# Kernel optimization log

Measured on AMD Instinct MI355X. Metric: run time of the kernel, lower is better.

## Reference

```python
import jax, jax.numpy as jnp
import numpy as np

D, H, C = 128, 128, 10
N, M, T = 256, 128, 128
DELTA = 1.0
SIGMA2 = 1.0
JITTER = 1e-3


def _net(params, x):
    # x: (D,) -> (C,)   2-hidden-layer tanh MLP (the `network` of NTKSVGP)
    W1, b1, W2, b2, W3, b3 = params
    h = jnp.tanh(x @ W1 + b1)
    h = jnp.tanh(h @ W2 + b2)
    return h @ W3 + b3


def _flat_jac(params, X):
    # per-sample jacobian wrt all params, flattened over params: (B, C, P)
    jac = jax.vmap(lambda x: jax.jacrev(_net)(params, x))(X)
    leaves = jax.tree_util.tree_leaves(jac)
    return jnp.concatenate([j.reshape(j.shape[0], j.shape[1], -1) for j in leaves], axis=-1)


def _forward(X, Y, Z, X_test, W1, b1, W2, b2, W3, b3):
    params = (W1, b1, W2, b2, W3, b3)
    scale = 1.0 / (DELTA * N)  # build_ntk: 1/(delta*num_data)

    Jx = _flat_jac(params, X)       # (N, C, P)
    Jz = _flat_jac(params, Z)       # (M, C, P)
    Jt = _flat_jac(params, X_test)  # (T, C, P)

    Kzx = jnp.einsum('mcp,ncp->cmn', Jz, Jx) * scale   # (C, M, N)
    Kzz = jnp.einsum('mcp,kcp->cmk', Jz, Jz) * scale   # (C, M, M)

    # Gaussian likelihood duals: beta = 2*Hessian = I/sigma2, alpha = -d nll/df = (Y-F)/sigma2
    F = jax.vmap(_net, in_axes=(None, 0))(params, X)   # (N, C)
    beta_diag = jnp.ones_like(F) / SIGMA2              # (N, C)
    alpha = (Y - F) / SIGMA2
    Lam = alpha + F * beta_diag                        # calc_lambda

    # beta_u = Kzx diag(beta) Kzx^T ; Lambda_u = Kzx Lambda
    beta_u = jnp.einsum('cmn,nc,ckn->cmk', Kzx, beta_diag, Kzx)  # (C, M, M)
    Lambda_u = jnp.einsum('cmn,nc->cm', Kzx, Lam)                # (C, M)

    Iz = jnp.eye(M, dtype=Kzz.dtype)
    Kzz_j = Kzz + JITTER * Iz
    KzzB = Kzz_j + beta_u + JITTER * Iz
    alpha_u = jnp.linalg.solve(KzzB, Lambda_u[..., None])[..., 0]  # (C, M)

    # predict_from_sparse_duals (full_cov=False branch)
    Lm = jnp.linalg.cholesky(Kzz_j)  # lower, batched over C
    Lb = jnp.linalg.cholesky(KzzB)
    Kxz = jnp.einsum('tcp,mcp->ctm', Jt, Jz) * scale  # (C, T, M)
    Kxx_diag = jnp.einsum('tcp,tcp->ct', Jt, Jt) * scale  # (C, T)

    f_mean = jnp.einsum('ctm,cm->tc', Kxz, alpha_u)   # (T, C)
    Kzxt = jnp.swapaxes(Kxz, -1, -2)                  # (C, M, T)
    Am = jax.scipy.linalg.solve_triangular(Lm, Kzxt, lower=True)
    Ab = jax.scipy.linalg.solve_triangular(Lb, Kzxt, lower=True)
    f_var = Kxx_diag - jnp.sum(Am * Am, axis=-2) + jnp.sum(Ab * Ab, axis=-2)  # (C, T)
    return jnp.stack([f_mean, f_var.T])  # (2, T, C)


def setup_inputs() -> dict:
    key = jax.random.key(0)
    ks = jax.random.split(key, 8)
    return {
        'X': jax.random.normal(ks[0], (N, D), jnp.float32),
        'Y': jax.random.normal(ks[1], (N, C), jnp.float32),
        'Z': jax.random.normal(ks[2], (M, D), jnp.float32),
        'X_test': jax.random.normal(ks[3], (T, D), jnp.float32),
        'W1': jax.random.normal(ks[4], (D, H), jnp.float32) / np.sqrt(D),
        'b1': jnp.zeros((H,), jnp.float32),
        'W2': jax.random.normal(ks[5], (H, H), jnp.float32) / np.sqrt(H),
        'b2': jnp.zeros((H,), jnp.float32),
        'W3': jax.random.normal(ks[6], (H, C), jnp.float32) / np.sqrt(H),
        'b3': jnp.zeros((C,), jnp.float32),
    }


def reference(X, Y, Z, X_test, W1, b1, W2, b2, W3, b3):
    return _forward(X, Y, Z, X_test, W1, b1, W2, b2, W3, b3)
```

## Files before the change

### kernel.cpp

```cpp
#include <hip/hip_runtime.h>

#define H 128
#define DD 128
#define CC 10
#define NX 256
#define MZ 128
#define TN 128
#define S_TOT 512
#define SCALE (1.0f/256.0f)
#define JIT 1e-3f
#define INV_S2 1.0f

#define OFF_XS    0u
#define OFF_A1    (OFF_XS   + S_TOT*DD)
#define OFF_A2    (OFF_A1   + S_TOT*H)
#define OFF_G1    (OFF_A2   + S_TOT*H)
#define OFF_G2    (OFF_G1   + S_TOT*CC*H)
#define OFF_W2T   (OFF_G2   + S_TOT*CC*H)
#define OFF_BASE  (OFF_W2T  + H*H)
#define BASE_ZX   0u
#define BASE_ZZ   (3u*MZ*NX)
#define BASE_TZ   (3u*MZ*NX + 3u*MZ*MZ)
#define OFF_KZX   (OFF_BASE + 3u*MZ*NX + 3u*MZ*MZ + 3u*TN*MZ)
#define OFF_KZZ   (OFF_KZX  + CC*MZ*NX)
#define OFF_KXZ   (OFF_KZZ  + CC*MZ*MZ)
#define OFF_KZZJ  (OFF_KXZ  + CC*TN*MZ)
#define OFF_KZZB  (OFF_KZZJ + CC*MZ*MZ)
#define OFF_LAMU  (OFF_KZZB + CC*MZ*MZ)
#define OFF_LC    (OFF_LAMU + CC*MZ)
#define OFF_INVD  (OFF_LC   + 2u*CC*MZ*MZ)
#define OFF_YLAM  (OFF_INVD + 2u*CC*MZ)

__global__ __launch_bounds__(128) void k_w2t(const float* __restrict__ W2, float* __restrict__ W2T,
                                             float* __restrict__ LamU) {
  int k = blockIdx.x, h = threadIdx.x;
  W2T[k*H + h] = W2[h*H + k];
  if (k < CC) LamU[k*MZ + h] = 0.0f;
}

__global__ __launch_bounds__(128) void k_features(
    const float* __restrict__ X, const float* __restrict__ Z, const float* __restrict__ Xt,
    const float* __restrict__ W1, const float* __restrict__ b1,
    const float* __restrict__ W2, const float* __restrict__ b2,
    const float* __restrict__ W3, const float* __restrict__ W2T,
    float* __restrict__ XS, float* __restrict__ A1, float* __restrict__ A2,
    float* __restrict__ G1, float* __restrict__ G2, float* __restrict__ out)
{
  int s = blockIdx.x, h = threadIdx.x;
  const float* xin = (s < NX) ? X + s*DD : (s < NX+MZ ? Z + (s-NX)*DD : Xt + (s-NX-MZ)*DD);
  __shared__ float xs[DD], a1s[H], g2s[CC*H];
  __shared__ float red[2];
  float xv = xin[h];
  xs[h] = xv; XS[s*DD + h] = xv;
  __syncthreads();
  float acc = b1[h];
  #pragma unroll 4
  for (int d0 = 0; d0 < DD; ++d0) acc += xs[d0] * W1[d0*H + h];
  float a1 = tanhf(acc);
  a1s[h] = a1; A1[s*H + h] = a1;
  __syncthreads();
  acc = b2[h];
  #pragma unroll 4
  for (int d0 = 0; d0 < H; ++d0) acc += a1s[d0] * W2[d0*H + h];
  float a2 = tanhf(acc);
  A2[s*H + h] = a2;
  float t2 = 1.0f - a2*a2;
  #pragma unroll
  for (int c = 0; c < CC; ++c) {
    float g2 = W3[h*CC + c] * t2;
    g2s[c*H + h] = g2;
    G2[(s*CC + c)*H + h] = g2;
  }
  __syncthreads();
  float t1 = 1.0f - a1*a1;
  float accs[CC];
  #pragma unroll
  for (int c = 0; c < CC; ++c) accs[c] = 0.0f;
  for (int k = 0; k < H; ++k) {
    float w = W2T[k*H + h];
    #pragma unroll
    for (int c = 0; c < CC; ++c) accs[c] += w * g2s[c*H + k];
  }
  #pragma unroll
  for (int c = 0; c < CC; ++c) G1[(s*CC + c)*H + h] = t1 * accs[c];
  if (s >= NX + MZ) {
    int t = s - NX - MZ;
    float v, nx, na1, na2;
    v = xv*xv;
    #pragma unroll
    for (int off = 32; off > 0; off >>= 1) v += __shfl_down(v, off, 64);
    if ((h & 63) == 0) red[h >> 6] = v;
    __syncthreads(); nx = red[0] + red[1]; __syncthreads();
    v = a1*a1;
    #pragma unroll
    for (int off = 32; off > 0; off >>= 1) v += __shfl_down(v, off, 64);
    if ((h & 63) == 0) red[h >> 6] = v;
    __syncthreads(); na1 = red[0] + red[1]; __syncthreads();
    v = a2*a2;
    #pragma unroll
    for (int off = 32; off > 0; off >>= 1) v += __shfl_down(v, off, 64);
    if ((h & 63) == 0) red[h >> 6] = v;
    __syncthreads(); na2 = red[0] + red[1]; __syncthreads();
    float base1 = 1.0f + nx, base2 = 1.0f + na1, base3 = 1.0f + na2;
    #pragma unroll
    for (int c = 0; c < CC; ++c) {
      float g1v = t1 * accs[c];
      float g2v = g2s[c*H + h];
      float n1, n2;
      v = g1v*g1v;
      #pragma unroll
      for (int off = 32; off > 0; off >>= 1) v += __shfl_down(v, off, 64);
      if ((h & 63) == 0) red[h >> 6] = v;
      __syncthreads(); n1 = red[0] + red[1]; __syncthreads();
      v = g2v*g2v;
      #pragma unroll
      for (int off = 32; off > 0; off >>= 1) v += __shfl_down(v, off, 64);
      if ((h & 63) == 0) red[h >> 6] = v;
      __syncthreads(); n2 = red[0] + red[1]; __syncthreads();
      if (h == 0) out[TN*CC + t*CC + c] = SCALE * (base1*n1 + base2*n2 + base3);
    }
  }
}

__global__ __launch_bounds__(256) void k_base(const float* __restrict__ XS,
    const float* __restrict__ A1, const float* __restrict__ A2, float* __restrict__ Base)
{
  int set = blockIdx.z;
  int colsN = (set == 0) ? NX : MZ;
  if ((int)blockIdx.x * 16 >= colsN) return;
  int rowOff = (set == 2) ? NX+MZ : NX;
  int colOff = (set == 0) ? 0 : NX;
  unsigned baseOff = (set == 0) ? BASE_ZX : (set == 1 ? BASE_ZZ : BASE_TZ);
  __shared__ float rx[16*132], r1[16*132], r2[16*132], cxs[16*132], c1s[16*132], c2s[16*132];
  int tid = threadIdx.x, m0 = blockIdx.y*16, n0 = blockIdx.x*16;
  for (int idx = tid; idx < 16*128; idx += 256) {
    int r = idx >> 7, hh = idx & 127;
    int sr = rowOff + m0 + r, sc = colOff + n0 + r;
    rx [r*132+hh] = XS[sr*DD+hh]; r1[r*132+hh] = A1[sr*H+hh]; r2[r*132+hh] = A2[sr*H+hh];
    cxs[r*132+hh] = XS[sc*DD+hh]; c1s[r*132+hh] = A1[sc*H+hh]; c2s[r*132+hh] = A2[sc*H+hh];
  }
  __syncthreads();
  int ty = tid >> 4, tx = tid & 15;
  const float4* pa = (const float4*)(rx  + ty*132);
  const float4* pb = (const float4*)(cxs + tx*132);
  const float4* pc = (const float4*)(r1  + ty*132);
  const float4* pd = (const float4*)(c1s + tx*132);
  const float4* pe = (const float4*)(r2  + ty*132);
  const float4* pf = (const float4*)(c2s + tx*132);
  float d0 = 0, d1 = 0, d2 = 0;
  #pragma unroll 8
  for (int q = 0; q < 32; ++q) {
    float4 a = pa[q], b = pb[q]; d0 += a.x*b.x + a.y*b.y + a.z*b.z + a.w*b.w;
    float4 c = pc[q], d = pd[q]; d1 += c.x*d.x + c.y*d.y + c.z*d.z + c.w*d.w;
    float4 e = pe[q], f = pf[q]; d2 += e.x*f.x + e.y*f.y + e.z*f.z + e.w*f.w;
  }
  int m = m0 + ty, n = n0 + tx;
  float* Bp = Base + baseOff;
  int area = 128 * colsN;
  Bp[0*area + m*colsN + n] = 1.0f + d0;
  Bp[1*area + m*colsN + n] = 1.0f + d1;
  Bp[2*area + m*colsN + n] = 1.0f + d2;
}

__global__ __launch_bounds__(256) void k_gram(const float* __restrict__ G1, const float* __restrict__ G2,
    const float* __restrict__ Base, const float* __restrict__ Y,
    float* __restrict__ Kzx, float* __restrict__ Kzz, float* __restrict__ Kxz,
    float* __restrict__ LamU)
{
  int z = blockIdx.z, set = z / CC, c = z % CC;
  int colsN = (set == 0) ? NX : MZ;
  if ((int)blockIdx.x * 16 >= colsN) return;
  int rowOff = (set == 2) ? NX+MZ : NX;
  int colOff = (set == 0) ? 0 : NX;
  unsigned baseOff = (set == 0) ? BASE_ZX : (set == 1 ? BASE_ZZ : BASE_TZ);
  float* outp = (set == 0) ? Kzx + c*MZ*NX : (set == 1 ? Kzz + c*MZ*MZ : Kxz + c*TN*MZ);
  __shared__ float g1r[16*132], g2r[16*132], g1c[16*132], g2c[16*132];
  int tid = threadIdx.x, m0 = blockIdx.y*16, n0 = blockIdx.x*16;
  for (int idx = tid; idx < 2048; idx += 256) {
    int r = idx >> 7, hh = idx & 127;
    int sr = rowOff + m0 + r, sc = colOff + n0 + r;
    g1r[r*132+hh] = G1[(sr*CC + c)*H + hh]; g2r[r*132+hh] = G2[(sr*CC + c)*H + hh];
    g1c[r*132+hh] = G1[(sc*CC + c)*H + hh]; g2c[r*132+hh] = G2[(sc*CC + c)*H + hh];
  }
  __syncthreads();
  int ty = tid >> 4, tx = tid & 15;
  const float4* p1 = (const float4*)(g1r + ty*132);
  const float4* p2 = (const float4*)(g1c + tx*132);
  const float4* p3 = (const float4*)(g2r + ty*132);
  const float4* p4 = (const float4*)(g2c + tx*132);
  float dg1 = 0, dg2 = 0;
  #pragma unroll 8
  for (int q = 0; q < 32; ++q) {
    float4 a = p1[q], b = p2[q]; dg1 += a.x*b.x + a.y*b.y + a.z*b.z + a.w*b.w;
    float4 e = p3[q], f = p4[q]; dg2 += e.x*f.x + e.y*f.y + e.z*f.z + e.w*f.w;
  }
  int m = m0 + ty, n = n0 + tx;
  const float* Bp = Base + baseOff;
  int area = 128 * colsN;
  float b0 = Bp[m*colsN + n], b1v = Bp[area + m*colsN + n], b2v = Bp[2*area + m*colsN + n];
  float val = SCALE * (b0*dg1 + b1v*dg2 + b2v);
  outp[m*colsN + n] = val;
  if (set == 0) {
    float lam = val * Y[n*CC + c] * INV_S2;
    lam += __shfl_xor(lam, 1, 64); lam += __shfl_xor(lam, 2, 64);
    lam += __shfl_xor(lam, 4, 64); lam += __shfl_xor(lam, 8, 64);
    if (tx == 0) atomicAdd(&LamU[c*MZ + m], lam);
  }
}

__global__ __launch_bounds__(256) void k_kzzb(const float* __restrict__ Kzx, const float* __restrict__ Kzz,
    float* __restrict__ Kzzj, float* __restrict__ KzzB)
{
  int c = blockIdx.z, m0 = blockIdx.y*16, k0 = blockIdx.x*16;
  int tid = threadIdx.x, ty = tid >> 4, tx = tid & 15;
  __shared__ float Am[16*17], Ak[16*17];
  const float* Kc = Kzx + c*MZ*NX;
  float acc = 0;
  for (int nc = 0; nc < NX; nc += 16) {
    Am[ty*17+tx] = Kc[(m0+ty)*NX + nc + tx];
    Ak[ty*17+tx] = Kc[(k0+ty)*NX + nc + tx];
    __syncthreads();
    #pragma unroll
    for (int p = 0; p < 16; ++p) acc += Am[ty*17+p] * Ak[tx*17+p];
    __syncthreads();
  }
  int m = m0+ty, k = k0+tx, idx = c*MZ*MZ + m*MZ + k;
  float kzz = Kzz[idx];
  float dia = (m == k) ? 1.0f : 0.0f;
  Kzzj[idx] = kzz + dia*JIT;
  KzzB[idx] = kzz + acc*INV_S2 + dia*2.0f*JIT;
}

__global__ __launch_bounds__(512) void k_chol(const float* __restrict__ Kzzj, const float* __restrict__ KzzB,
    float* __restrict__ Lc, float* __restrict__ invd,
    const float* __restrict__ LamU, float* __restrict__ ylam)
{
  int which = blockIdx.x & 1, c = blockIdx.x >> 1;
  const float* Ain = (which ? KzzB : Kzzj) + c*MZ*MZ;
  float* LcB = Lc + (size_t)(which*CC + c)*MZ*MZ;
  float* invB = invd + (which*CC + c)*MZ;
  __shared__ float As[MZ*MZ];
  __shared__ float4 pan[MZ];
  __shared__ float bs[MZ];
  __shared__ float ys[MZ];
  int tid = threadIdx.x;
  int rg = tid & 31, kp = tid >> 5;
  float4* As4 = (float4*)As;
  {
    float4* d4 = (float4*)As; const float4* s4 = (const float4*)Ain;
    #pragma unroll
    for (int r = 0; r < 8; ++r) d4[tid + 512*r] = s4[tid + 512*r];
  }
  if (tid < MZ) bs[tid] = which ? LamU[c*MZ + tid] : 0.0f;
  __syncthreads();
  for (int jb = 0; jb < 32; ++jb) {
    int j = jb*4;
    if (tid < MZ) {
      int i = tid;
      float r0 = As[(j+0)*MZ + i], r1 = As[(j+1)*MZ + i], r2 = As[(j+2)*MZ + i], r3 = As[(j+3)*MZ + i];
      float a00 = As[j*MZ+j];
      float a10 = As[j*MZ+j+1], a20 = As[j*MZ+j+2], a30 = As[j*MZ+j+3];
      float a11 = As[(j+1)*MZ+j+1], a21 = As[(j+1)*MZ+j+2], a31 = As[(j+1)*MZ+j+3];
      float a22 = As[(j+2)*MZ+j+2], a32 = As[(j+2)*MZ+j+3];
      float a33 = As[(j+3)*MZ+j+3];
      float bj0 = bs[j], bj1 = bs[j+1], bj2 = bs[j+2], bj3 = bs[j+3];
      float id0 = rsqrtf(a00);
      float l10 = a10*id0, l20 = a20*id0, l30 = a30*id0;
      float id1 = rsqrtf(a11 - l10*l10);
      float l21 = (a21 - l20*l10)*id1, l31 = (a31 - l30*l10)*id1;
      float id2 = rsqrtf(a22 - l20*l20 - l21*l21);
      float l32 = (a32 - l30*l20 - l31*l21)*id2;
      float id3 = rsqrtf(a33 - l30*l30 - l31*l31 - l32*l32);
      float c0 = r0*id0;
      float c1 = (r1 - c0*l10)*id1;
      float c2 = (r2 - c0*l20 - c1*l21)*id2;
      float c3 = (r3 - c0*l30 - c1*l31 - c2*l32)*id3;
      float y0 = bj0*id0;
      float y1 = (bj1 - l10*y0)*id1;
      float y2 = (bj2 - l20*y0 - l21*y1)*id2;
      float y3 = (bj3 - l30*y0 - l31*y1 - l32*y2)*id3;
      pan[i] = make_float4(c0, c1, c2, c3);
      LcB[(j+0)*MZ + i] = (i > j+0) ? c0 : 0.0f;
      LcB[(j+1)*MZ + i] = (i > j+1) ? c1 : 0.0f;
      LcB[(j+2)*MZ + i] = (i > j+2) ? c2 : 0.0f;
      LcB[(j+3)*MZ + i] = (i > j+3) ? c3 : 0.0f;
      if (i == j) {
        invB[j] = id0; invB[j+1] = id1; invB[j+2] = id2; invB[j+3] = id3;
        ys[j] = y0; ys[j+1] = y1; ys[j+2] = y2; ys[j+3] = y3;
      }
      if (i >= j+4) bs[i] -= c0*y0 + c1*y1 + c2*y2 + c3*y3;
    }
    __syncthreads();
    float4 p0 = pan[4*rg+0], p1 = pan[4*rg+1], p2 = pan[4*rg+2], p3 = pan[4*rg+3];
    int kstart = (j + 4) + ((kp - (j + 4)) & 15);
    int kend = 4*rg + 3;
    for (int k = kstart; k <= kend; k += 16) {
      float4 ck = pan[k];
      float4 a4 = As4[k*32 + rg];
      a4.x -= p0.x*ck.x + p0.y*ck.y + p0.z*ck.z + p0.w*ck.w;
      a4.y -= p1.x*ck.x + p1.y*ck.y + p1.z*ck.z + p1.w*ck.w;
      a4.z -= p2.x*ck.x + p2.y*ck.y + p2.z*ck.z + p2.w*ck.w;
      a4.w -= p3.x*ck.x + p3.y*ck.y + p3.z*ck.z + p3.w*ck.w;
      As4[k*32 + rg] = a4;
    }
    __syncthreads();
  }
  if (which && tid < MZ) ylam[c*MZ + tid] = ys[tid];
}

__device__ __forceinline__ float rdlane(float v, int lane) {
  return __int_as_float(__builtin_amdgcn_readlane(__float_as_int(v), lane));
}

__global__ __launch_bounds__(512) void k_solve(const float* __restrict__ Lc,
    const float* __restrict__ invd, const float* __restrict__ ylam,
    const float* __restrict__ Kxz, float* __restrict__ out)
{
  int quarter = blockIdx.x & 3;
  int which   = (blockIdx.x >> 2) & 1;
  int c       = blockIdx.x >> 3;
  const float2* LcB2 = (const float2*)(Lc + (size_t)(which*CC + c)*MZ*MZ);
  const float2* invB2 = (const float2*)(invd + (which*CC + c)*MZ);
  const float2* ylB2  = (const float2*)(ylam + c*MZ);
  int tid = threadIdx.x, l = tid & 63, wv = tid >> 6;
  __shared__ float2 Ls[MZ*64];
  #pragma unroll
  for (int r = 0; r < 16; ++r) Ls[tid + 512*r] = LcB2[tid + 512*r];
  float2 iv = invB2[l];
  float2 yl = ylB2[l];
  int col0 = quarter*32 + wv*4;
  const float* K0 = Kxz + (size_t)c*TN*MZ;
  float2 b0 = *(const float2*)(K0 + (size_t)(col0+0)*MZ + 2*l);
  float2 b1 = *(const float2*)(K0 + (size_t)(col0+1)*MZ + 2*l);
  float2 b2 = *(const float2*)(K0 + (size_t)(col0+2)*MZ + 2*l);
  float2 b3 = *(const float2*)(K0 + (size_t)(col0+3)*MZ + 2*l);
  __syncthreads();
  #pragma unroll
  for (int j = 0; j < MZ; ++j) {
    const int owner = j >> 1;
    float2 Lj = Ls[j*64 + l];
    float y0, y1, y2, y3;
    if ((j & 1) == 0) {
      y0 = rdlane(b0.x * iv.x, owner);
      y1 = rdlane(b1.x * iv.x, owner);
      y2 = rdlane(b2.x * iv.x, owner);
      y3 = rdlane(b3.x * iv.x, owner);
    } else {
      y0 = rdlane(b0.y * iv.y, owner);
      y1 = rdlane(b1.y * iv.y, owner);
      y2 = rdlane(b2.y * iv.y, owner);
      y3 = rdlane(b3.y * iv.y, owner);
    }
    b0.x -= Lj.x * y0; b0.y -= Lj.y * y0;
    b1.x -= Lj.x * y1; b1.y -= Lj.y * y1;
    b2.x -= Lj.x * y2; b2.y -= Lj.y * y2;
    b3.x -= Lj.x * y3; b3.y -= Lj.y * y3;
    if (l == owner) {
      if ((j & 1) == 0) { b0.x = y0; b1.x = y1; b2.x = y2; b3.x = y3; }
      else              { b0.y = y0; b1.y = y1; b2.y = y2; b3.y = y3; }
    }
  }
  float sq0 = b0.x*b0.x + b0.y*b0.y, fm0 = b0.x*yl.x + b0.y*yl.y;
  float sq1 = b1.x*b1.x + b1.y*b1.y, fm1 = b1.x*yl.x + b1.y*yl.y;
  float sq2 = b2.x*b2.x + b2.y*b2.y, fm2 = b2.x*yl.x + b2.y*yl.y;
  float sq3 = b3.x*b3.x + b3.y*b3.y, fm3 = b3.x*yl.x + b3.y*yl.y;
  #pragma unroll
  for (int off = 32; off > 0; off >>= 1) {
    sq0 += __shfl_xor(sq0, off, 64); fm0 += __shfl_xor(fm0, off, 64);
    sq1 += __shfl_xor(sq1, off, 64); fm1 += __shfl_xor(fm1, off, 64);
    sq2 += __shfl_xor(sq2, off, 64); fm2 += __shfl_xor(fm2, off, 64);
    sq3 += __shfl_xor(sq3, off, 64); fm3 += __shfl_xor(fm3, off, 64);
  }
  if (l == 0) {
    float sgn = which ? 1.0f : -1.0f;
    float* var = out + TN*CC;
    atomicAdd(&var[(col0+0)*CC + c], sgn*sq0);
    atomicAdd(&var[(col0+1)*CC + c], sgn*sq1);
    atomicAdd(&var[(col0+2)*CC + c], sgn*sq2);
    atomicAdd(&var[(col0+3)*CC + c], sgn*sq3);
    if (which) {
      out[(col0+0)*CC + c] = fm0;
      out[(col0+1)*CC + c] = fm1;
      out[(col0+2)*CC + c] = fm2;
      out[(col0+3)*CC + c] = fm3;
    }
  }
}

extern "C" void kernel_launch(void* const* d_in, const int* in_sizes, int n_in,
                              void* d_out, int out_size, void* d_ws, size_t ws_size,
                              hipStream_t stream) {
  (void)in_sizes; (void)n_in; (void)out_size; (void)ws_size;
  const float* X  = (const float*)d_in[0];
  const float* Y  = (const float*)d_in[1];
  const float* Z  = (const float*)d_in[2];
  const float* Xt = (const float*)d_in[3];
  const float* W1 = (const float*)d_in[4];
  const float* b1 = (const float*)d_in[5];
  const float* W2 = (const float*)d_in[6];
  const float* b2 = (const float*)d_in[7];
  const float* W3 = (const float*)d_in[8];
  float* ws  = (float*)d_ws;
  float* out = (float*)d_out;

  float* XS   = ws + OFF_XS;
  float* A1   = ws + OFF_A1;
  float* A2   = ws + OFF_A2;
  float* G1   = ws + OFF_G1;
  float* G2   = ws + OFF_G2;
  float* W2T  = ws + OFF_W2T;
  float* Base = ws + OFF_BASE;
  float* Kzx  = ws + OFF_KZX;
  float* Kzz  = ws + OFF_KZZ;
  float* Kxz  = ws + OFF_KXZ;
  float* Kzzj = ws + OFF_KZZJ;
  float* KzzB = ws + OFF_KZZB;
  float* LamU = ws + OFF_LAMU;
  float* Lc   = ws + OFF_LC;
  float* invd = ws + OFF_INVD;
  float* ylam = ws + OFF_YLAM;

  k_w2t<<<128, 128, 0, stream>>>(W2, W2T, LamU);
  k_features<<<S_TOT, 128, 0, stream>>>(X, Z, Xt, W1, b1, W2, b2, W3, W2T, XS, A1, A2, G1, G2, out);
  k_base<<<dim3(16, 8, 3), 256, 0, stream>>>(XS, A1, A2, Base);
  k_gram<<<dim3(16, 8, 3*CC), 256, 0, stream>>>(G1, G2, Base, Y, Kzx, Kzz, Kxz, LamU);
  k_kzzb<<<dim3(8, 8, CC), 256, 0, stream>>>(Kzx, Kzz, Kzzj, KzzB);
  k_chol<<<2*CC, 512, 0, stream>>>(Kzzj, KzzB, Lc, invd, LamU, ylam);
  k_solve<<<8*CC, 512, 0, stream>>>(Lc, invd, ylam, Kxz, out);
}
```

Baseline: 137.1 us.

## Fuse all pipeline stages into one cooperative kernel with grid syncs

```diff
diff --git a/kernel.cpp b/kernel.cpp
--- a/kernel.cpp
+++ b/kernel.cpp
@@ -1,4 +1,6 @@
 #include <hip/hip_runtime.h>
+#include <hip/hip_cooperative_groups.h>
+namespace cg = cooperative_groups;
 
 #define H 128
 #define DD 128
@@ -30,6 +32,384 @@
 #define OFF_LC    (OFF_LAMU + CC*MZ)
 #define OFF_INVD  (OFF_LC   + 2u*CC*MZ*MZ)
 #define OFF_YLAM  (OFF_INVD + 2u*CC*MZ)
+
+__device__ __forceinline__ float rdlane(float v, int lane) {
+  return __int_as_float(__builtin_amdgcn_readlane(__float_as_int(v), lane));
+}
+
+#define WRED(val, qi) { float v_ = (val);                                     \
+  v_ += __shfl_down(v_,32,64); v_ += __shfl_down(v_,16,64);                   \
+  v_ += __shfl_down(v_, 8,64); v_ += __shfl_down(v_, 4,64);                   \
+  v_ += __shfl_down(v_, 2,64); v_ += __shfl_down(v_, 1,64);                   \
+  if ((h & 63) == 0) partG[(qi)*2 + (h>>6)] = v_; }
+
+__global__ __launch_bounds__(512) void mega(
+    const float* __restrict__ X, const float* __restrict__ Y,
+    const float* __restrict__ Z, const float* __restrict__ Xt,
+    const float* __restrict__ W1, const float* __restrict__ b1v_,
+    const float* __restrict__ W2, const float* __restrict__ b2v_,
+    const float* __restrict__ W3, float* __restrict__ ws, float* __restrict__ out)
+{
+  cg::grid_group grid = cg::this_grid();
+  __shared__ float4 smem4[4288];
+  float* SM = (float*)smem4;
+  int tid = threadIdx.x;
+  int b = blockIdx.x;
+
+  float* XS  = ws + OFF_XS;
+  float* A1  = ws + OFF_A1;
+  float* A2  = ws + OFF_A2;
+  float* G1  = ws + OFF_G1;
+  float* G2  = ws + OFF_G2;
+  float* Base= ws + OFF_BASE;
+  float* Kzx = ws + OFF_KZX;
+  float* Kzz = ws + OFF_KZZ;
+  float* Kxz = ws + OFF_KXZ;
+  float* Kzzj= ws + OFF_KZZJ;
+  float* KzzB= ws + OFF_KZZB;
+  float* LamU= ws + OFF_LAMU;
+  float* Lc  = ws + OFF_LC;
+  float* invd= ws + OFF_INVD;
+  float* ylam= ws + OFF_YLAM;
+
+  {
+    if (b == 0) for (int i = tid; i < CC*MZ; i += 512) LamU[i] = 0.0f;
+    int g = tid >> 7, h = tid & 127;
+    bool act = (tid < 256);
+    int s = 2*b + g;
+    float* xs    = SM + g*1600;
+    float* a1s   = xs + 128;
+    float* g2s   = a1s + 128;
+    float* partG = SM + 3200 + g*46;
+    const float* xin = (s < NX) ? X + s*DD : (s < NX+MZ ? Z + (s-NX)*DD : Xt + (s-NX-MZ)*DD);
+    float xv=0, a1=0, a2=0, t1=0, t2=0, acc;
+    float accs[CC], g2v[CC];
+    if (act) { xv = xin[h]; xs[h] = xv; XS[s*DD+h] = xv; }
+    __syncthreads();
+    if (act) {
+      acc = b1v_[h];
+      #pragma unroll 4
+      for (int d0 = 0; d0 < DD; ++d0) acc += xs[d0]*W1[d0*H+h];
+      a1 = tanhf(acc); a1s[h] = a1; A1[s*H+h] = a1;
+    }
+    __syncthreads();
+    if (act) {
+      acc = b2v_[h];
+      #pragma unroll 4
+      for (int d0 = 0; d0 < H; ++d0) acc += a1s[d0]*W2[d0*H+h];
+      a2 = tanhf(acc); A2[s*H+h] = a2;
+      t2 = 1.0f - a2*a2;
+      #pragma unroll
+      for (int c = 0; c < CC; ++c) {
+        g2v[c] = W3[h*CC+c]*t2; g2s[c*H+h] = g2v[c]; G2[(s*CC+c)*H+h] = g2v[c];
+      }
+    }
+    __syncthreads();
+    if (act) {
+      t1 = 1.0f - a1*a1;
+      #pragma unroll
+      for (int c = 0; c < CC; ++c) accs[c] = 0.0f;
+      const float4* w2r = (const float4*)(W2 + h*H);
+      for (int k4 = 0; k4 < 32; ++k4) {
+        float4 wv = w2r[k4]; int k = 4*k4;
+        #pragma unroll
+        for (int c = 0; c < CC; ++c)
+          accs[c] += wv.x*g2s[c*H+k] + wv.y*g2s[c*H+k+1] + wv.z*g2s[c*H+k+2] + wv.w*g2s[c*H+k+3];
+      }
+      #pragma unroll
+      for (int c = 0; c < CC; ++c) G1[(s*CC+c)*H+h] = t1*accs[c];
+    }
+    if (b >= 192) {
+      if (act) {
+        WRED(xv*xv, 0) WRED(a1*a1, 1) WRED(a2*a2, 2)
+        #pragma unroll
+        for (int c = 0; c < CC; ++c) {
+          float g1v = t1*accs[c];
+          WRED(g1v*g1v, 3+2*c)
+          WRED(g2v[c]*g2v[c], 4+2*c)
+        }
+      }
+      __syncthreads();
+      if (tid < 2*CC) {
+        int gi = tid / CC, c = tid % CC;
+        const float* P = SM + 3200 + gi*46;
+        float nx = P[0]+P[1], na1 = P[2]+P[3], na2 = P[4]+P[5];
+        float n1 = P[(3+2*c)*2] + P[(3+2*c)*2+1];
+        float n2 = P[(4+2*c)*2] + P[(4+2*c)*2+1];
+        int t = 2*(b-192) + gi;
+        out[TN*CC + t*CC + c] = SCALE*((1.0f+nx)*n1 + (1.0f+na1)*n2 + (1.0f+na2));
+      }
+    }
+  }
+  grid.sync();
+
+  {
+    int set, m0, n0;
+    if (b < 128)      { set = 0; m0 = (b>>4)*16;              n0 = (b&15)*16; }
+    else if (b < 192) { set = 1; int v = b-128; m0 = (v>>3)*16; n0 = (v&7)*16; }
+    else              { set = 2; int v = b-192; m0 = (v>>3)*16; n0 = (v&7)*16; }
+    int colsN = (set == 0) ? NX : MZ;
+    int rowOff = (set == 2) ? NX+MZ : NX;
+    int colOff = (set == 0) ? 0 : NX;
+    unsigned baseOff = (set == 0) ? BASE_ZX : (set == 1 ? BASE_ZZ : BASE_TZ);
+    float *rx = SM, *r1 = SM+2112, *r2 = SM+4224, *cxs = SM+6336, *c1s = SM+8448, *c2s = SM+10560;
+    for (int idx = tid; idx < 2048; idx += 512) {
+      int r = idx >> 7, hh = idx & 127;
+      int sr = rowOff + m0 + r, sc = colOff + n0 + r;
+      rx [r*132+hh] = XS[sr*DD+hh]; r1[r*132+hh] = A1[sr*H+hh]; r2[r*132+hh] = A2[sr*H+hh];
+      cxs[r*132+hh] = XS[sc*DD+hh]; c1s[r*132+hh] = A1[sc*H+hh]; c2s[r*132+hh] = A2[sc*H+hh];
+    }
+    __syncthreads();
+    if (tid < 256) {
+      int ty = tid >> 4, tx = tid & 15;
+      const float4* pa = (const float4*)(rx  + ty*132);
+      const float4* pb = (const float4*)(cxs + tx*132);
+      const float4* pc = (const float4*)(r1  + ty*132);
+      const float4* pd = (const float4*)(c1s + tx*132);
+      const float4* pe = (const float4*)(r2  + ty*132);
+      const float4* pf = (const float4*)(c2s + tx*132);
+      float d0 = 0, d1 = 0, d2 = 0;
+      #pragma unroll 8
+      for (int q = 0; q < 32; ++q) {
+        float4 a = pa[q], bb = pb[q]; d0 += a.x*bb.x + a.y*bb.y + a.z*bb.z + a.w*bb.w;
+        float4 c = pc[q], d = pd[q];  d1 += c.x*d.x + c.y*d.y + c.z*d.z + c.w*d.w;
+        float4 e = pe[q], f = pf[q];  d2 += e.x*f.x + e.y*f.y + e.z*f.z + e.w*f.w;
+      }
+      int m = m0 + ty, n = n0 + tx;
+      float* Bp = Base + baseOff;
+      int area = 128 * colsN;
+      Bp[0*area + m*colsN + n] = 1.0f + d0;
+      Bp[1*area + m*colsN + n] = 1.0f + d1;
+      Bp[2*area + m*colsN + n] = 1.0f + d2;
+    }
+  }
+  grid.sync();
+
+  {
+    float *g1r = SM, *g2r = SM+2112, *g1c = SM+4224, *g2c = SM+6336;
+    for (int u = b; u < 3840; u += 256) {
+      int z = u >> 7, rem = u & 127, m0 = (rem>>4)*16, n0 = (rem&15)*16;
+      int set = z / CC, c = z % CC;
+      int colsN = (set == 0) ? NX : MZ;
+      if (n0 >= colsN) continue;
+      int rowOff = (set == 2) ? NX+MZ : NX;
+      int colOff = (set == 0) ? 0 : NX;
+      unsigned baseOff = (set == 0) ? BASE_ZX : (set == 1 ? BASE_ZZ : BASE_TZ);
+      float* outp = (set == 0) ? Kzx + c*MZ*NX : (set == 1 ? Kzz + c*MZ*MZ : Kxz + c*TN*MZ);
+      for (int idx = tid; idx < 2048; idx += 512) {
+        int r = idx >> 7, hh = idx & 127;
+        int sr = rowOff + m0 + r, sc = colOff + n0 + r;
+        g1r[r*132+hh] = G1[(sr*CC+c)*H+hh]; g2r[r*132+hh] = G2[(sr*CC+c)*H+hh];
+        g1c[r*132+hh] = G1[(sc*CC+c)*H+hh]; g2c[r*132+hh] = G2[(sc*CC+c)*H+hh];
+      }
+      __syncthreads();
+      if (tid < 256) {
+        int ty = tid >> 4, tx = tid & 15;
+        const float4* p1 = (const float4*)(g1r + ty*132);
+        const float4* p2 = (const float4*)(g1c + tx*132);
+        const float4* p3 = (const float4*)(g2r + ty*132);
+        const float4* p4 = (const float4*)(g2c + tx*132);
+        float dg1 = 0, dg2 = 0;
+        #pragma unroll 8
+        for (int q = 0; q < 32; ++q) {
+          float4 a = p1[q], bb = p2[q]; dg1 += a.x*bb.x + a.y*bb.y + a.z*bb.z + a.w*bb.w;
+          float4 e = p3[q], f = p4[q];  dg2 += e.x*f.x + e.y*f.y + e.z*f.z + e.w*f.w;
+        }
+        int m = m0 + ty, n = n0 + tx;
+        const float* Bp = Base + baseOff;
+        int area = 128 * colsN;
+        float bb0 = Bp[m*colsN+n], bb1 = Bp[area+m*colsN+n], bb2 = Bp[2*area+m*colsN+n];
+        float val = SCALE * (bb0*dg1 + bb1*dg2 + bb2);
+        outp[m*colsN + n] = val;
+        if (set == 0) {
+          float lam = val * Y[n*CC + c] * INV_S2;
+          lam += __shfl_xor(lam, 1, 64); lam += __shfl_xor(lam, 2, 64);
+          lam += __shfl_xor(lam, 4, 64); lam += __shfl_xor(lam, 8, 64);
+          if (tx == 0) atomicAdd(&LamU[c*MZ + m], lam);
+        }
+      }
+      __syncthreads();
+    }
+  }
+  grid.sync();
+
+  {
+    float* Am = SM; float* Ak = SM + 272;
+    for (int u = b; u < 640; u += 256) {
+      int c = u >> 6, rem = u & 63, m0 = (rem>>3)*16, k0 = (rem&7)*16;
+      const float* Kc = Kzx + c*MZ*NX;
+      int ty = tid >> 4, tx = tid & 15;
+      float acc = 0;
+      for (int nc = 0; nc < NX; nc += 16) {
+        if (tid < 256) {
+          Am[ty*17+tx] = Kc[(m0+ty)*NX + nc + tx];
+          Ak[ty*17+tx] = Kc[(k0+ty)*NX + nc + tx];
+        }
+        __syncthreads();
+        if (tid < 256) {
+          #pragma unroll
+          for (int p = 0; p < 16; ++p) acc += Am[ty*17+p] * Ak[tx*17+p];
+        }
+        __syncthreads();
+      }
+      if (tid < 256) {
+        int m = m0+ty, k = k0+tx, idx = c*MZ*MZ + m*MZ + k;
+        float kzz = Kzz[idx];
+        float dia = (m == k) ? 1.0f : 0.0f;
+        Kzzj[idx] = kzz + dia*JIT;
+        KzzB[idx] = kzz + acc*INV_S2 + dia*2.0f*JIT;
+      }
+      __syncthreads();
+    }
+  }
+  grid.sync();
+
+  if (b < 20) {
+    int which = b & 1, c = b >> 1;
+    const float* Ain = (which ? KzzB : Kzzj) + c*MZ*MZ;
+    float* LcB = Lc + (size_t)(which*CC + c)*MZ*MZ;
+    float* invB = invd + (which*CC + c)*MZ;
+    float* As = SM;
+    float4* pan = smem4 + 4096;
+    float* bs = SM + 16896;
+    float* ys = SM + 17024;
+    float4* As4 = (float4*)As;
+    {
+      float4* d4 = (float4*)As; const float4* s4 = (const float4*)Ain;
+      #pragma unroll
+      for (int r = 0; r < 8; ++r) d4[tid + 512*r] = s4[tid + 512*r];
+    }
+    if (tid < MZ) bs[tid] = which ? LamU[c*MZ + tid] : 0.0f;
+    __syncthreads();
+    int rg = tid & 31, kp = tid >> 5;
+    for (int jb = 0; jb < 32; ++jb) {
+      int j = jb*4;
+      if (tid < MZ) {
+        int i = tid;
+        float r0 = As[(j+0)*MZ+i], r1 = As[(j+1)*MZ+i], r2 = As[(j+2)*MZ+i], r3 = As[(j+3)*MZ+i];
+        float a00 = As[j*MZ+j];
+        float a10 = As[j*MZ+j+1], a20 = As[j*MZ+j+2], a30 = As[j*MZ+j+3];
+        float a11 = As[(j+1)*MZ+j+1], a21 = As[(j+1)*MZ+j+2], a31 = As[(j+1)*MZ+j+3];
+        float a22 = As[(j+2)*MZ+j+2], a32 = As[(j+2)*MZ+j+3];
+        float a33 = As[(j+3)*MZ+j+3];
+        float bj0 = bs[j], bj1 = bs[j+1], bj2 = bs[j+2], bj3 = bs[j+3];
+        float id0 = rsqrtf(a00);
+        float l10 = a10*id0, l20 = a20*id0, l30 = a30*id0;
+        float id1 = rsqrtf(a11 - l10*l10);
+        float l21 = (a21 - l20*l10)*id1, l31 = (a31 - l30*l10)*id1;
+        float id2 = rsqrtf(a22 - l20*l20 - l21*l21);
+        float l32 = (a32 - l30*l20 - l31*l21)*id2;
+        float id3 = rsqrtf(a33 - l30*l30 - l31*l31 - l32*l32);
+        float c0 = r0*id0;
+        float c1 = (r1 - c0*l10)*id1;
+        float c2 = (r2 - c0*l20 - c1*l21)*id2;
+        float c3 = (r3 - c0*l30 - c1*l31 - c2*l32)*id3;
+        float y0 = bj0*id0;
+        float y1 = (bj1 - l10*y0)*id1;
+        float y2 = (bj2 - l20*y0 - l21*y1)*id2;
+        float y3 = (bj3 - l30*y0 - l31*y1 - l32*y2)*id3;
+        pan[i] = make_float4(c0, c1, c2, c3);
+        LcB[(j+0)*MZ+i] = (i > j+0) ? c0 : 0.0f;
+        LcB[(j+1)*MZ+i] = (i > j+1) ? c1 : 0.0f;
+        LcB[(j+2)*MZ+i] = (i > j+2) ? c2 : 0.0f;
+        LcB[(j+3)*MZ+i] = (i > j+3) ? c3 : 0.0f;
+        if (i == j) {
+          invB[j] = id0; invB[j+1] = id1; invB[j+2] = id2; invB[j+3] = id3;
+          ys[j] = y0; ys[j+1] = y1; ys[j+2] = y2; ys[j+3] = y3;
+        }
+        if (i >= j+4) bs[i] -= c0*y0 + c1*y1 + c2*y2 + c3*y3;
+      }
+      __syncthreads();
+      float4 p0 = pan[4*rg+0], p1 = pan[4*rg+1], p2 = pan[4*rg+2], p3 = pan[4*rg+3];
+      int kstart = (j + 4) + ((kp - (j + 4)) & 15);
+      int kend = 4*rg + 3;
+      for (int k = kstart; k <= kend; k += 16) {
+        float4 ck = pan[k];
+        float4 a4 = As4[k*32 + rg];
+        a4.x -= p0.x*ck.x + p0.y*ck.y + p0.z*ck.z + p0.w*ck.w;
+        a4.y -= p1.x*ck.x + p1.y*ck.y + p1.z*ck.z + p1.w*ck.w;
+        a4.z -= p2.x*ck.x + p2.y*ck.y + p2.z*ck.z + p2.w*ck.w;
+        a4.w -= p3.x*ck.x + p3.y*ck.y + p3.z*ck.z + p3.w*ck.w;
+        As4[k*32 + rg] = a4;
+      }
+      __syncthreads();
+    }
+    if (which && tid < MZ) ylam[c*MZ + tid] = ys[tid];
+  }
+  grid.sync();
+
+  if (b < 80) {
+    int quarter = b & 3;
+    int which   = (b >> 2) & 1;
+    int c       = b >> 3;
+    const float2* LcB2 = (const float2*)(Lc + (size_t)(which*CC + c)*MZ*MZ);
+    const float2* invB2 = (const float2*)(invd + (which*CC + c)*MZ);
+    const float2* ylB2  = (const float2*)(ylam + c*MZ);
+    int l = tid & 63, wv2 = tid >> 6;
+    float2* Ls = (float2*)SM;
+    #pragma unroll
+    for (int r = 0; r < 16; ++r) Ls[tid + 512*r] = LcB2[tid + 512*r];
+    float2 iv = invB2[l];
+    float2 yl = ylB2[l];
+    int col0 = quarter*32 + wv2*4;
+    const float* K0 = Kxz + (size_t)c*TN*MZ;
+    float2 b0 = *(const float2*)(K0 + (size_t)(col0+0)*MZ + 2*l);
+    float2 b1 = *(const float2*)(K0 + (size_t)(col0+1)*MZ + 2*l);
+    float2 b2 = *(const float2*)(K0 + (size_t)(col0+2)*MZ + 2*l);
+    float2 b3 = *(const float2*)(K0 + (size_t)(col0+3)*MZ + 2*l);
+    __syncthreads();
+    #pragma unroll
+    for (int j = 0; j < MZ; ++j) {
+      const int owner = j >> 1;
+      float2 Lj = Ls[j*64 + l];
+      float y0, y1, y2, y3;
+      if ((j & 1) == 0) {
+        y0 = rdlane(b0.x * iv.x, owner);
+        y1 = rdlane(b1.x * iv.x, owner);
+        y2 = rdlane(b2.x * iv.x, owner);
+        y3 = rdlane(b3.x * iv.x, owner);
+      } else {
+        y0 = rdlane(b0.y * iv.y, owner);
+        y1 = rdlane(b1.y * iv.y, owner);
+        y2 = rdlane(b2.y * iv.y, owner);
+        y3 = rdlane(b3.y * iv.y, owner);
+      }
+      b0.x -= Lj.x * y0; b0.y -= Lj.y * y0;
+      b1.x -= Lj.x * y1; b1.y -= Lj.y * y1;
+      b2.x -= Lj.x * y2; b2.y -= Lj.y * y2;
+      b3.x -= Lj.x * y3; b3.y -= Lj.y * y3;
+      if (l == owner) {
+        if ((j & 1) == 0) { b0.x = y0; b1.x = y1; b2.x = y2; b3.x = y3; }
+        else              { b0.y = y0; b1.y = y1; b2.y = y2; b3.y = y3; }
+      }
+    }
+    float sq0 = b0.x*b0.x + b0.y*b0.y, fm0 = b0.x*yl.x + b0.y*yl.y;
+    float sq1 = b1.x*b1.x + b1.y*b1.y, fm1 = b1.x*yl.x + b1.y*yl.y;
+    float sq2 = b2.x*b2.x + b2.y*b2.y, fm2 = b2.x*yl.x + b2.y*yl.y;
+    float sq3 = b3.x*b3.x + b3.y*b3.y, fm3 = b3.x*yl.x + b3.y*yl.y;
+    #pragma unroll
+    for (int off = 32; off > 0; off >>= 1) {
+      sq0 += __shfl_xor(sq0, off, 64); fm0 += __shfl_xor(fm0, off, 64);
+      sq1 += __shfl_xor(sq1, off, 64); fm1 += __shfl_xor(fm1, off, 64);
+      sq2 += __shfl_xor(sq2, off, 64); fm2 += __shfl_xor(fm2, off, 64);
+      sq3 += __shfl_xor(sq3, off, 64); fm3 += __shfl_xor(fm3, off, 64);
+    }
+    if (l == 0) {
+      float sgn = which ? 1.0f : -1.0f;
+      float* var = out + TN*CC;
+      atomicAdd(&var[(col0+0)*CC + c], sgn*sq0);
+      atomicAdd(&var[(col0+1)*CC + c], sgn*sq1);
+      atomicAdd(&var[(col0+2)*CC + c], sgn*sq2);
+      atomicAdd(&var[(col0+3)*CC + c], sgn*sq3);
+      if (which) {
+        out[(col0+0)*CC + c] = fm0;
+        out[(col0+1)*CC + c] = fm1;
+        out[(col0+2)*CC + c] = fm2;
+        out[(col0+3)*CC + c] = fm3;
+      }
+    }
+  }
+}
 
 __global__ __launch_bounds__(128) void k_w2t(const float* __restrict__ W2, float* __restrict__ W2T,
                                              float* __restrict__ LamU) {
@@ -306,10 +686,6 @@
     __syncthreads();
   }
   if (which && tid < MZ) ylam[c*MZ + tid] = ys[tid];
-}
-
-__device__ __forceinline__ float rdlane(float v, int lane) {
-  return __int_as_float(__builtin_amdgcn_readlane(__float_as_int(v), lane));
 }
 
 __global__ __launch_bounds__(512) void k_solve(const float* __restrict__ Lc,
@@ -403,6 +779,12 @@
   float* ws  = (float*)d_ws;
   float* out = (float*)d_out;
 
+  void* margs[] = {(void*)&X, (void*)&Y, (void*)&Z, (void*)&Xt, (void*)&W1, (void*)&b1,
+                   (void*)&W2, (void*)&b2, (void*)&W3, (void*)&ws, (void*)&out};
+  hipError_t e = hipLaunchCooperativeKernel((const void*)mega, dim3(256), dim3(512),
+                                            margs, 0, stream);
+  if (e == hipSuccess) return;
+
   float* XS   = ws + OFF_XS;
   float* A1   = ws + OFF_A1;
   float* A2   = ws + OFF_A2;
```

After: 314.3 us. 129% more time.
